# Performance work log

Measured on AMD Instinct MI355X. Metric: run time of the kernel, lower is better.

Reference implementation:

```python
import jax, jax.numpy as jnp
import numpy as np

B, C, H, W = 32, 128, 64, 64
D = 256          # attn_unit_dim
FF = 512         # ffn latent dim (2.0 * 256, rounded to /16*16)
NL = 2           # n_attn_blocks
PH = PW = 2      # patch size
EPS = 1e-5


def _cf_ln(x, g, b):
    # channel-first LayerNorm over dim 1 (unbiased=False variance)
    m = jnp.mean(x, axis=1, keepdims=True)
    v = jnp.mean((x - m) ** 2, axis=1, keepdims=True)
    return (x - m) * jax.lax.rsqrt(v + EPS) * g.reshape(1, -1, 1, 1) + b.reshape(1, -1, 1, 1)


def _conv1x1(x, w, b=None):
    y = jnp.einsum('bcpq,dc->bdpq', x, w)
    return y if b is None else y + b.reshape(1, -1, 1, 1)


def _bn(x, g, b, m, v):
    # eval-mode BatchNorm2d with running stats
    return (x - m.reshape(1, -1, 1, 1)) * jax.lax.rsqrt(v.reshape(1, -1, 1, 1) + EPS) \
        * g.reshape(1, -1, 1, 1) + b.reshape(1, -1, 1, 1)


def setup_inputs() -> dict:
    key = jax.random.key(0)
    ks = iter(jax.random.split(key, 64))
    rn = lambda shape, s=0.02: jax.random.normal(next(ks), shape, jnp.float32) * s
    pv = lambda shape: 1.0 + 0.1 * jax.random.uniform(next(ks), shape, jnp.float32)
    return {
        'x': jax.random.normal(next(ks), (B, C, H, W), jnp.float32),
        # local_rep: depthwise 3x3 + BN + leaky_relu, then 1x1 -> D
        'dw_w': rn((C, 1, 3, 3), 0.1),
        'bn1_g': pv((C,)), 'bn1_b': rn((C,), 0.1),
        'bn1_m': rn((C,), 0.1), 'bn1_v': pv((C,)),
        'c1_w': rn((D, C)), 'c1_b': rn((D,), 0.01),
        # per-layer transformer params (stacked over NL)
        'ln1_g': pv((NL, D)), 'ln1_b': rn((NL, D), 0.1),
        'qkv_w': rn((NL, 1 + 2 * D, D)), 'qkv_b': rn((NL, 1 + 2 * D), 0.01),
        'out_w': rn((NL, D, D)), 'out_b': rn((NL, D), 0.01),
        'ln2_g': pv((NL, D)), 'ln2_b': rn((NL, D), 0.1),
        'f1_w': rn((NL, FF, D)), 'f1_b': rn((NL, FF), 0.01),
        'f2_w': rn((NL, D, FF)), 'f2_b': rn((NL, D), 0.01),
        'lnf_g': pv((D,)), 'lnf_b': rn((D,), 0.1),
        # conv_proj: 1x1 (no bias) + BN
        'proj_w': rn((C, D)),
        'bn2_g': pv((C,)), 'bn2_b': rn((C,), 0.1),
        'bn2_m': rn((C,), 0.1), 'bn2_v': pv((C,)),
    }


def reference(x, dw_w, bn1_g, bn1_b, bn1_m, bn1_v, c1_w, c1_b,
              ln1_g, ln1_b, qkv_w, qkv_b, out_w, out_b,
              ln2_g, ln2_b, f1_w, f1_b, f2_w, f2_b,
              lnf_g, lnf_b, proj_w, bn2_g, bn2_b, bn2_m, bn2_v):
    # local representation: depthwise 3x3 conv + BN + leaky_relu(0.1) + 1x1 conv
    y = jax.lax.conv_general_dilated(
        x, dw_w, window_strides=(1, 1), padding=[(1, 1), (1, 1)],
        dimension_numbers=('NCHW', 'OIHW', 'NCHW'), feature_group_count=C)
    y = _bn(y, bn1_g, bn1_b, bn1_m, bn1_v)
    y = jax.nn.leaky_relu(y, 0.1)
    y = _conv1x1(y, c1_w, c1_b)                       # [B, D, H, W]

    # unfold -> [B, D, P, N], P = PH*PW pixels/patch, N = patches
    nh, nw = H // PH, W // PW
    p = y.reshape(B, D, nh, PH, nw, PW).transpose(0, 1, 3, 5, 2, 4).reshape(B, D, PH * PW, nh * nw)

    # global representation: NL pre-norm linear-attention transformer blocks
    for l in range(NL):
        z = _cf_ln(p, ln1_g[l], ln1_b[l])
        qkv = _conv1x1(z, qkv_w[l], qkv_b[l])          # [B, 1+2D, P, N]
        q, k, v = qkv[:, :1], qkv[:, 1:1 + D], qkv[:, 1 + D:]
        scores = jax.nn.softmax(q, axis=-1)            # softmax over patches N
        ctx = jnp.sum(k * scores, axis=-1, keepdims=True)  # [B, D, P, 1]
        attn = _conv1x1(jax.nn.relu(v) * ctx, out_w[l], out_b[l])
        p = p + attn
        z = _cf_ln(p, ln2_g[l], ln2_b[l])
        h = jax.nn.leaky_relu(_conv1x1(z, f1_w[l], f1_b[l]), 0.1)
        p = p + _conv1x1(h, f2_w[l], f2_b[l])
    p = _cf_ln(p, lnf_g, lnf_b)

    # fold back -> [B, D, H, W]
    fm = p.reshape(B, D, PH, PW, nh, nw).transpose(0, 1, 4, 2, 5, 3).reshape(B, D, H, W)

    # conv_proj: 1x1 (no bias) + BN -> [B, C, H, W]
    fm = _conv1x1(fm, proj_w)
    fm = _bn(fm, bn2_g, bn2_b, bn2_m, bn2_v)
    return fm
```

## Files before the change

kernel.cpp:

```cpp
#include <hip/hip_runtime.h>


typedef short  bh8 __attribute__((ext_vector_type(8)));
typedef float  f4  __attribute__((ext_vector_type(4)));
typedef unsigned short us2 __attribute__((ext_vector_type(2)));
typedef unsigned short us4 __attribute__((ext_vector_type(4)));

constexpr int Bc = 32, Cc = 128, Dc = 256, FFc = 512;
constexpr int NNc = 1024, Sc = 4096;
constexpr float EPSc = 1e-5f;

enum SrcMode { S_LNF32, S_BF16 };
enum OutMode { O_STOREF32, O_FOLDBN };

__device__ __forceinline__ unsigned short f2bf(float f) {
  union { float f; unsigned int u; } v; v.f = f;
  unsigned int u = v.u + 0x7FFFu + ((v.u >> 16) & 1u);
  return (unsigned short)(u >> 16);
}

__global__ __launch_bounds__(256) void k_wconv(
    const float* __restrict__ w, unsigned short* __restrict__ dst,
    int total, int klog2)
{
// ... 49 lines not shown
  *reinterpret_cast<us2*>(y1 + base + (ph * 2 + 0) * NNc) = (us2){r[0], r[2]};
  *reinterpret_cast<us2*>(y1 + base + (ph * 2 + 1) * NNc) = (us2){r[1], r[3]};
}

template<bool QD>
__global__ __launch_bounds__(256) void k_lnstats(
    const float* __restrict__ p, const float* __restrict__ wgq,
    float* __restrict__ mean_, float* __restrict__ rstd_, float* __restrict__ qdot)
{
  __shared__ float wg_s[256];
  int t = threadIdx.x;
  if (QD) { wg_s[t] = wgq[t]; __syncthreads(); }
  int pos = blockIdx.x * 256 + t;
  int b = pos >> 12, s = pos & 4095;
  const float* base = p + (size_t)b * Dc * Sc + s;
  float sum = 0.f, sq = 0.f, qa = 0.f;
  for (int d = 0; d < Dc; ++d) {
    float v = base[(size_t)d * Sc];
    sum += v; sq += v * v;
    if (QD) qa += v * wg_s[d];
  }
  float m   = sum * (1.f / Dc);
  float var = sq * (1.f / Dc) - m * m;
  mean_[pos] = m;
  rstd_[pos] = rsqrtf(fmaxf(var, 0.f) + EPSc);
  if (QD) qdot[pos] = qa;
}

__global__ void k_prep(const float* __restrict__ wq, const float* __restrict__ lng,
                       const float* __restrict__ lnb, const float* __restrict__ qb,
                       float* __restrict__ wgq, float* __restrict__ scal)
{
  int t = threadIdx.x, lane = t & 63, wv = t >> 6;
  float w = wq[t];
  float a = w * lng[t], c2 = w * lnb[t];
  wgq[t] = a;
  __shared__ float ra[4], rb[4];
  #pragma unroll
  for (int off = 32; off > 0; off >>= 1) { a += __shfl_xor(a, off); c2 += __shfl_xor(c2, off); }
  if (lane == 0) { ra[wv] = a; rb[wv] = c2; }
  __syncthreads();
  if (t == 0) {
    scal[0] = ra[0] + ra[1] + ra[2] + ra[3];
    scal[1] = rb[0] + rb[1] + rb[2] + rb[3] + qb[0];
  }
}

__global__ __launch_bounds__(256) void k_softmax2(
    const float* __restrict__ qdot, const float* __restrict__ mean_,
    const float* __restrict__ rstd_, const float* __restrict__ scal,
    float* __restrict__ ub, float* __restrict__ Ub)
{
  int bp = blockIdx.x, b = bp >> 2, pp = bp & 3;
  int t = threadIdx.x, lane = t & 63, wv = t >> 6;
  __shared__ float r3[4], r4[4];
  float s1 = scal[0], s2 = scal[1];
  int pos0 = b * Sc + pp * NNc;
  float q[4], m_r[4], rs_r[4];
  float mx = -3.4e38f;
  #pragma unroll
  for (int i = 0; i < 4; ++i) {
    int pos = pos0 + t + i * 256;
    m_r[i] = mean_[pos]; rs_r[i] = rstd_[pos];
    q[i] = rs_r[i] * qdot[pos] - m_r[i] * rs_r[i] * s1 + s2;
    mx = fmaxf(mx, q[i]);
  }
  #pragma unroll
  for (int off = 32; off > 0; off >>= 1) mx = fmaxf(mx, __shfl_xor(mx, off));
  if (lane == 0) r3[wv] = mx;
  __syncthreads();
  mx = fmaxf(fmaxf(r3[0], r3[1]), fmaxf(r3[2], r3[3]));
  float sum = 0.f;
  #pragma unroll
  for (int i = 0; i < 4; ++i) { q[i] = __expf(q[i] - mx); sum += q[i]; }
  #pragma unroll
  for (int off = 32; off > 0; off >>= 1) sum += __shfl_xor(sum, off);
  if (lane == 0) r4[wv] = sum;
  __syncthreads();
  float inv = 1.f / (r4[0] + r4[1] + r4[2] + r4[3]);
  float pU = 0.f;
  #pragma unroll
  for (int i = 0; i < 4; ++i) {
    float un = rs_r[i] * q[i] * inv;
    ub[(size_t)bp * NNc + t + i * 256] = un;
    pU += m_r[i] * un;
  }
  #pragma unroll
  for (int off = 32; off > 0; off >>= 1) pU += __shfl_xor(pU, off);
  if (lane == 0) r3[wv] = pU;
  __syncthreads();
  if (t == 0) Ub[bp] = r3[0] + r3[1] + r3[2] + r3[3];
}

__global__ __launch_bounds__(256) void k_tpass(
    const float* __restrict__ p, const float* __restrict__ ub,
    const float* __restrict__ Ub, const float* __restrict__ lng,
    const float* __restrict__ lnb, float* __restrict__ tb)
{
  int cs = blockIdx.x, pp = blockIdx.y, b = blockIdx.z;
  int bp = b * 4 + pp;
  int t = threadIdx.x, lane = t & 63, wv = t >> 6;
  __shared__ float u_s[1024];
  for (int i = t; i < 1024; i += 256) u_s[i] = ub[(size_t)bp * NNc + i];
  __syncthreads();
  float U = Ub[bp];
  const float* pb = p + (size_t)b * Dc * Sc + pp * NNc;
  for (int i = 0; i < 16; ++i) {
    int c = cs * 64 + wv * 16 + i;
    const float* row = pb + (size_t)c * Sc;
    float sm = 0.f;
    #pragma unroll
    for (int j = 0; j < 16; ++j) { int n = lane + 64 * j; sm += row[n] * u_s[n]; }
    #pragma unroll
    for (int off = 32; off > 0; off >>= 1) sm += __shfl_xor(sm, off);
    if (lane == 0) tb[(size_t)bp * Dc + c] = lng[c] * (sm - U) + lnb[c];
  }
}

__global__ __launch_bounds__(256) void k_ctx2(
    const float* __restrict__ tb, const float* __restrict__ wk,
    const float* __restrict__ bk, float* __restrict__ ctxb)
{
  int b = blockIdx.x, d = threadIdx.x;
  __shared__ float ts[4][256];
  for (int i = threadIdx.x; i < 1024; i += 256) ts[i >> 8][i & 255] = tb[(size_t)b * 1024 + i];
  __syncthreads();
  const float* wrow = wk + (size_t)d * 256;
  float bkd = bk[d];
  float accp[4] = {0.f, 0.f, 0.f, 0.f};
  for (int c = 0; c < 256; c += 4) {
    float4 wv = *reinterpret_cast<const float4*>(wrow + c);
    #pragma unroll
    for (int pp = 0; pp < 4; ++pp)
      accp[pp] += wv.x * ts[pp][c] + wv.y * ts[pp][c + 1]
                + wv.z * ts[pp][c + 2] + wv.w * ts[pp][c + 3];
  }
  #pragma unroll
  for (int pp = 0; pp < 4; ++pp)
    ctxb[((size_t)(b * 256 + d)) * 4 + pp] = accp[pp] + bkd;
}

__global__ void k_bn2pre(const float* __restrict__ g, const float* __restrict__ bb,
                         const float* __restrict__ mm, const float* __restrict__ vv,
                         float* __restrict__ sc, float* __restrict__ sh)
{
  int c = threadIdx.x;
  if (c < Cc) {
    float s = g[c] * rsqrtf(vv[c] + EPSc);
    sc[c] = s;
    sh[c] = bb[c] - mm[c] * s;
  }
}

template<int M1, bool ATTN, bool QDOT>
__global__ __launch_bounds__(256) void k_fused(
    const float* __restrict__ p,
    const float* __restrict__ mean_, const float* __restrict__ rstd_,
    const float* __restrict__ lng, const float* __restrict__ lnb,
    const unsigned short* __restrict__ wf1, const float* __restrict__ b1,
    const float* __restrict__ ctxp,
    const unsigned short* __restrict__ wf2, const float* __restrict__ b2,
    float* __restrict__ dst,
    const float* __restrict__ wgq2,
    float* __restrict__ mean_o, float* __restrict__ rstd_o,
    float* __restrict__ qdot_o)
{
  constexpr int NT = 32;
  constexpr int NF = NT / 16;
  constexpr int ACC1 = M1 / 64;
  int t = threadIdx.x;
  int wv = t >> 6, lane = t & 63;
  int q = lane >> 4, ln16 = lane & 15;
  int nt = blockIdx.x, pp = blockIdx.y, b = blockIdx.z;
  int n0 = nt * NT;

  __shared__ unsigned int Alds[2][NT * 20];
  __shared__ unsigned short Frag[M1 * NT];
  __shared__ float m_s[NT], rs_s[NT];
  __shared__ float ctx_s[ATTN ? 256 : 4];

  int kp_s = t >> 4;
  int n2_s = (t & 15) * 2;

  size_t pbase = (size_t)b * Dc * Sc + pp * NNc + n0;

  float2 c0 = *reinterpret_cast<const float2*>(p + pbase + (size_t)(kp_s * 2) * Sc + n2_s);
  float2 c1 = *reinterpret_cast<const float2*>(p + pbase + (size_t)(kp_s * 2 + 1) * Sc + n2_s);

  if (t < NT) {
    int pos = b * Sc + pp * NNc + n0 + t;
    m_s[t]  = mean_[pos];
    rs_s[t] = rstd_[pos];
  }
  if (ATTN) ctx_s[t] = ctxp[(size_t)(b * Dc + t) * 4 + pp];

  f4 acc[ACC1][NF];
  #pragma unroll
  for (int i = 0; i < ACC1; ++i)
    #pragma unroll
    for (int j = 0; j < NF; ++j) acc[i][j] = (f4){0.f, 0.f, 0.f, 0.f};

  __syncthreads();

  for (int kc = 0; kc < 256; kc += 32) {
    int k0 = kc + kp_s * 2;
    float g0 = lng[k0], g1 = lng[k0 + 1];
    float h0 = lnb[k0], h1 = lnb[k0 + 1];
    float ms0 = m_s[n2_s],     rs0 = rs_s[n2_s];
    float ms1 = m_s[n2_s + 1], rs1 = rs_s[n2_s + 1];
    float a00 = (c0.x - ms0) * rs0 * g0 + h0;
    float a01 = (c0.y - ms1) * rs1 * g0 + h0;
    float a10 = (c1.x - ms0) * rs0 * g1 + h1;
    float a11 = (c1.y - ms1) * rs1 * g1 + h1;
    unsigned int pk0 = (unsigned int)f2bf(a00) | ((unsigned int)f2bf(a10) << 16);
    unsigned int pk1 = (unsigned int)f2bf(a01) | ((unsigned int)f2bf(a11) << 16);

    if (kc < 224) {
      c0 = *reinterpret_cast<const float2*>(p + pbase + (size_t)(kc + 32 + kp_s * 2) * Sc + n2_s);
      c1 = *reinterpret_cast<const float2*>(p + pbase + (size_t)(kc + 32 + kp_s * 2 + 1) * Sc + n2_s);
    }

    unsigned int* alw = Alds[(kc >> 5) & 1];
    alw[n2_s * 20 + kp_s]       = pk0;
    alw[(n2_s + 1) * 20 + kp_s] = pk1;

    bh8 aw[ACC1];
    #pragma unroll
    for (int tm = 0; tm < ACC1; ++tm)
      aw[tm] = *(const bh8*)(wf1 + ((size_t)((kc >> 5) * (M1 >> 4) + wv * ACC1 + tm) * 64 + lane) * 8);

    __syncthreads();

    const unsigned short* al = (const unsigned short*)Alds[(kc >> 5) & 1];
    #pragma unroll
    for (int tn = 0; tn < NF; ++tn) {
      bh8 bwf = *(const bh8*)(al + (tn * 16 + ln16) * 40 + q * 8);
      #pragma unroll
      for (int tm = 0; tm < ACC1; ++tm)
        acc[tm][tn] = __builtin_amdgcn_mfma_f32_16x16x32_bf16(aw[tm], bwf, acc[tm][tn], 0, 0, 0);
    }
  }

  #pragma unroll
  for (int tm = 0; tm < ACC1; ++tm) {
    int row0 = wv * (M1 / 4) + tm * 16 + q * 4;
    float bia[4], cxv[4];
    #pragma unroll
    for (int r = 0; r < 4; ++r) {
      bia[r] = b1[row0 + r];
      if (ATTN) cxv[r] = ctx_s[row0 + r];
    }
    int kt  = row0 >> 5;
    int sub = (row0 >> 3) & 3;
    int jo  = row0 & 7;
    #pragma unroll
    for (int tn = 0; tn < NF; ++tn) {
      int cl = tn * 16 + ln16;
      us4 pk;
      #pragma unroll
      for (int r = 0; r < 4; ++r) {
        float v = acc[tm][tn][r] + bia[r];
        if (ATTN) v = fmaxf(v, 0.f) * cxv[r];
        else      v = v > 0.f ? v : 0.1f * v;
        pk[r] = f2bf(v);
      }
      *reinterpret_cast<us4*>(Frag + (((kt * NF + (cl >> 4)) * 64 + (sub << 4 | (cl & 15))) * 8 + jo)) = pk;
    }
  }
  __syncthreads();

  f4 acc2[4][NF];
  #pragma unroll
  for (int i = 0; i < 4; ++i)
    #pragma unroll
    for (int j = 0; j < NF; ++j) acc2[i][j] = (f4){0.f, 0.f, 0.f, 0.f};

  for (int kc = 0; kc < M1; kc += 32) {
    bh8 aw2[4];
    #pragma unroll
    for (int tm = 0; tm < 4; ++tm)
      aw2[tm] = *(const bh8*)(wf2 + ((size_t)((kc >> 5) * 16 + wv * 4 + tm) * 64 + lane) * 8);
    #pragma unroll
    for (int tn = 0; tn < NF; ++tn) {
      bh8 bwf = *(const bh8*)(Frag + ((kc >> 5) * NF + tn) * 512 + lane * 8);
      #pragma unroll
      for (int tm = 0; tm < 4; ++tm)
        acc2[tm][tn] = __builtin_amdgcn_mfma_f32_16x16x32_bf16(aw2[tm], bwf, acc2[tm][tn], 0, 0, 0);
    }
  }

  float s1[NF], s2[NF], s3[NF];
  #pragma unroll
  for (int tn = 0; tn < NF; ++tn) { s1[tn] = 0.f; s2[tn] = 0.f; s3[tn] = 0.f; }
  #pragma unroll
  for (int tm = 0; tm < 4; ++tm) {
    #pragma unroll
    for (int r = 0; r < 4; ++r) {
      int row = wv * 64 + tm * 16 + q * 4 + r;
      float bv = b2[row];
      float wqr = QDOT ? wgq2[row] : 0.f;
      #pragma unroll
      for (int tn = 0; tn < NF; ++tn) {
        int col = n0 + tn * 16 + ln16;
        size_t da = (size_t)(b * Dc + row) * Sc + pp * NNc + col;
        float v = dst[da] + acc2[tm][tn][r] + bv;
        dst[da] = v;
        s1[tn] += v; s2[tn] += v * v;
        if (QDOT) s3[tn] += v * wqr;
      }
    }
  }
  #pragma unroll
  for (int tn = 0; tn < NF; ++tn) {
    s1[tn] += __shfl_xor(s1[tn], 16); s1[tn] += __shfl_xor(s1[tn], 32);
    s2[tn] += __shfl_xor(s2[tn], 16); s2[tn] += __shfl_xor(s2[tn], 32);
    if (QDOT) { s3[tn] += __shfl_xor(s3[tn], 16); s3[tn] += __shfl_xor(s3[tn], 32); }
  }
  __syncthreads();
  float* fr = (float*)Frag;
  if (q == 0) {
    #pragma unroll
    for (int tn = 0; tn < NF; ++tn) {
      int col = tn * 16 + ln16;
      fr[(wv * 3 + 0) * NT + col] = s1[tn];
      fr[(wv * 3 + 1) * NT + col] = s2[tn];
      fr[(wv * 3 + 2) * NT + col] = s3[tn];
    }
  }
  __syncthreads();
  if (t < NT) {
    float a1 = 0.f, a2 = 0.f, a3 = 0.f;
    #pragma unroll
    for (int w2 = 0; w2 < 4; ++w2) {
      a1 += fr[(w2 * 3 + 0) * NT + t];
      a2 += fr[(w2 * 3 + 1) * NT + t];
      a3 += fr[(w2 * 3 + 2) * NT + t];
    }
    int pos = b * Sc + pp * NNc + n0 + t;
    float mn  = a1 * (1.f / 256.f);
    float var = a2 * (1.f / 256.f) - mn * mn;
    mean_o[pos] = mn;
    rstd_o[pos] = rsqrtf(fmaxf(var, 0.f) + EPSc);
    if (QDOT) qdot_o[pos] = a3;
  }
}

template<int KTOT, int MTOT, int SRCCH, int SSTR, bool SPP,
         SrcMode SM, OutMode OM>
__global__ __launch_bounds__(256) void k_mm(
    const void* __restrict__ src,
    const float* __restrict__ mean_, const float* __restrict__ rstd_,
    const float* __restrict__ lng, const float* __restrict__ lnb,
    const unsigned short* __restrict__ wf, const float* __restrict__ bias,
    const float* __restrict__ bnsc, const float* __restrict__ bnsh,
    void* __restrict__ dst)
{
  int t = threadIdx.x;
  int wv = t >> 6, lane = t & 63;
  int wm = wv & 1, wn = wv >> 1;
  int q = lane >> 4, ln16 = lane & 15;
  int nb = blockIdx.x, b = blockIdx.z;
  int pp = blockIdx.y & 3, mb = blockIdx.y >> 2;
  int n0  = nb * 128;
  int MB0 = mb * 128;

  __shared__ unsigned int Alds[128 * 20];
  __shared__ float m_s[128], rs_s[128];

  if (SM == S_LNF32 && t < 128) {
    int pos = b * Sc + pp * NNc + n0 + t;
    m_s[t]  = mean_[pos];
    rs_s[t] = rstd_[pos];
  }

  f4 acc[4][4];
  #pragma unroll
  for (int i = 0; i < 4; ++i)
    #pragma unroll
    for (int j = 0; j < 4; ++j) acc[i][j] = (f4){0.f, 0.f, 0.f, 0.f};

  size_t sbase = (size_t)b * SRCCH * SSTR + pp * NNc + n0;
  int mtb = (MB0 >> 4) + wm * 4;

  for (int kc = 0; kc < KTOT; kc += 32) {
    bh8 aw[4];
    #pragma unroll
    for (int tm = 0; tm < 4; ++tm)
      aw[tm] = *(const bh8*)(wf + ((size_t)((kc >> 5) * (MTOT >> 4) + mtb + tm) * 64 + lane) * 8);
    __syncthreads();
    #pragma unroll
    for (int it = 0; it < 8; ++it) {
      int n_l = (t & 63) + (it & 1) * 64;
      int kp  = (t >> 6) + (it >> 1) * 4;
      int k0  = kc + kp * 2;
      unsigned int pk;
      if (SM == S_LNF32) {
        const float* sp = (const float*)src;
        float a0 = sp[sbase + (size_t)k0 * SSTR + n_l];
        float a1 = sp[sbase + (size_t)(k0 + 1) * SSTR + n_l];
        float ms = m_s[n_l], rs = rs_s[n_l];
        a0 = (a0 - ms) * rs * lng[k0] + lnb[k0];
        a1 = (a1 - ms) * rs * lng[k0 + 1] + lnb[k0 + 1];
        pk = (unsigned int)f2bf(a0) | ((unsigned int)f2bf(a1) << 16);
      } else {
        const unsigned short* sp = (const unsigned short*)src;
        unsigned int u0 = sp[sbase + (size_t)k0 * SSTR + n_l];
        unsigned int u1 = sp[sbase + (size_t)(k0 + 1) * SSTR + n_l];
        pk = u0 | (u1 << 16);
      }
      Alds[n_l * 20 + kp] = pk;
    }
    __syncthreads();
    const unsigned short* al = (const unsigned short*)Alds;
    #pragma unroll
    for (int tn = 0; tn < 4; ++tn) {
      int nrow = wn * 64 + tn * 16 + ln16;
      bh8 bwf = *(const bh8*)(al + nrow * 40 + q * 8);
      #pragma unroll
      for (int tm = 0; tm < 4; ++tm)
        acc[tm][tn] = __builtin_amdgcn_mfma_f32_16x16x32_bf16(aw[tm], bwf, acc[tm][tn], 0, 0, 0);
    }
  }

  #pragma unroll
  for (int tm = 0; tm < 4; ++tm) {
    #pragma unroll
    for (int r = 0; r < 4; ++r) {
      int row = MB0 + wm * 64 + tm * 16 + q * 4 + r;
      float scv = 0.f, shv = 0.f, bv = 0.f;
      if (OM == O_FOLDBN) { scv = bnsc[row]; shv = bnsh[row]; }
      else                { bv = bias[row]; }
      #pragma unroll
      for (int tn = 0; tn < 4; ++tn) {
        int col = n0 + wn * 64 + tn * 16 + ln16;
        float v = acc[tm][tn][r];
        if (OM == O_FOLDBN) {
          int hh = 2 * (col >> 5) + (pp >> 1), ww = 2 * (col & 31) + (pp & 1);
          ((float*)dst)[((size_t)(b * Cc + row)) * Sc + hh * 64 + ww] = v * scv + shv;
        } else {
          ((float*)dst)[(size_t)(b * MTOT + row) * Sc + pp * NNc + col] = v + bv;
        }
      }
    }
  }
}

extern "C" void kernel_launch(void* const* d_in, const int* in_sizes, int n_in,
                              void* d_out, int out_size, void* d_ws, size_t ws_size,
                              hipStream_t stream)
{
  const float* x     = (const float*)d_in[0];
  const float* dw_w  = (const float*)d_in[1];
  const float* bn1_g = (const float*)d_in[2];
  const float* bn1_b = (const float*)d_in[3];
  const float* bn1_m = (const float*)d_in[4];
  const float* bn1_v = (const float*)d_in[5];
  const float* c1_w  = (const float*)d_in[6];
  const float* c1_b  = (const float*)d_in[7];
  const float* ln1_g = (const float*)d_in[8];
  const float* ln1_b = (const float*)d_in[9];
  const float* qkv_w = (const float*)d_in[10];
  const float* qkv_b = (const float*)d_in[11];
  const float* out_w = (const float*)d_in[12];
  const float* out_b = (const float*)d_in[13];
  const float* ln2_g = (const float*)d_in[14];
  const float* ln2_b = (const float*)d_in[15];
  const float* f1_w  = (const float*)d_in[16];
  const float* f1_b  = (const float*)d_in[17];
  const float* f2_w  = (const float*)d_in[18];
  const float* f2_b  = (const float*)d_in[19];
  const float* lnf_g = (const float*)d_in[20];
  const float* lnf_b = (const float*)d_in[21];
  const float* projw = (const float*)d_in[22];
  const float* bn2_g = (const float*)d_in[23];
  const float* bn2_b = (const float*)d_in[24];
  const float* bn2_m = (const float*)d_in[25];
  const float* bn2_v = (const float*)d_in[26];
  float* out = (float*)d_out;

  float* ws    = (float*)d_ws;
  float* p     = ws;
  float* reg   = p + (size_t)33554432;
  unsigned short* y1u = (unsigned short*)reg;
  float* mean2 = reg;
  float* rstd2 = reg + 131072;
  float* meanb = reg   + (size_t)8388608;
  float* rstdb = meanb + 131072;
  float* qdotb = rstdb + 131072;
  float* ub    = qdotb + 131072;
  float* Ub    = ub    + 131072;
  float* tb    = Ub    + 128;
  float* ctxb  = tb    + 32768;
  float* wgq   = ctxb  + 32768;
  float* scal  = wgq   + 512;
  float* bnscb = scal  + 16;
  float* bnshb = bnscb + 128;
  unsigned short* wfb = (unsigned short*)(bnshb + 128);
  unsigned short* wf_c1   = wfb;
  unsigned short* wf_v0   = wfb + 32768;
  unsigned short* wf_proj = wfb + 32768 + 2 * 393216;

  k_wconv<<<128, 256, 0, stream>>>(c1_w, wf_c1, 256 * 128, 7);
  for (int l = 0; l < 2; ++l) {
    const float* wvp = qkv_w + ((size_t)l * 513 + 257) * Dc;
    unsigned short* base = wf_v0 + (size_t)l * 393216;
    k_wconv<<<256, 256, 0, stream>>>(wvp, base, 256 * 256, 8);
    k_wconv<<<256, 256, 0, stream>>>(out_w + (size_t)l * Dc * Dc, base + 65536, 256 * 256, 8);
    k_wconv<<<512, 256, 0, stream>>>(f1_w + (size_t)l * FFc * Dc, base + 131072, 512 * 256, 8);
    k_wconv<<<512, 256, 0, stream>>>(f2_w + (size_t)l * Dc * FFc, base + 262144, 256 * 512, 9);
  }
  k_wconv<<<128, 256, 0, stream>>>(projw, wf_proj, 128 * 256, 8);

  for (int l = 0; l < 2; ++l)
    k_prep<<<1, 256, 0, stream>>>(qkv_w + (size_t)l * 513 * Dc,
                                  ln1_g + l * Dc, ln1_b + l * Dc,
                                  qkv_b + l * 513, wgq + l * 256, scal + l * 2);

  k_dwconv<<<16384, 256, 0, stream>>>(x, dw_w, bn1_g, bn1_b, bn1_m, bn1_v, y1u);

  k_mm<128, 256, 128, 4096, true, S_BF16, O_STOREF32>
      <<<dim3(8, 8, 32), 256, 0, stream>>>(
      y1u, nullptr, nullptr, nullptr, nullptr, wf_c1, c1_b, nullptr, nullptr, p);

  k_lnstats<true><<<512, 256, 0, stream>>>(p, wgq, meanb, rstdb, qdotb);

  for (int l = 0; l < 2; ++l) {
    const float* g1 = ln1_g + l * Dc; const float* b1 = ln1_b + l * Dc;
    const float* g2 = ln2_g + l * Dc; const float* b2 = ln2_b + l * Dc;
    const float* wk = qkv_w + ((size_t)l * 513 + 1) * Dc;
    const float* bk = qkv_b + l * 513 + 1;
    const float* bvv = qkv_b + l * 513 + 257;
    unsigned short* wbase = wf_v0 + (size_t)l * 393216;

    k_softmax2<<<128, 256, 0, stream>>>(qdotb, meanb, rstdb, scal + l * 2, ub, Ub);
    k_tpass<<<dim3(4, 4, 32), 256, 0, stream>>>(p, ub, Ub, g1, b1, tb);
    k_ctx2<<<32, 256, 0, stream>>>(tb, wk, bk, ctxb);

    k_fused<256, true, false><<<dim3(32, 4, 32), 256, 0, stream>>>(
        p, meanb, rstdb, g1, b1, wbase, bvv, ctxb,
        wbase + 65536, out_b + l * Dc, p,
        nullptr, mean2, rstd2, nullptr);

    if (l == 0) {
      k_fused<512, false, true><<<dim3(32, 4, 32), 256, 0, stream>>>(
          p, mean2, rstd2, g2, b2, wbase + 131072, f1_b + l * FFc, nullptr,
          wbase + 262144, f2_b + l * Dc, p,
          wgq + 256, meanb, rstdb, qdotb);
    } else {
      k_fused<512, false, false><<<dim3(32, 4, 32), 256, 0, stream>>>(
          p, mean2, rstd2, g2, b2, wbase + 131072, f1_b + l * FFc, nullptr,
          wbase + 262144, f2_b + l * Dc, p,
          nullptr, meanb, rstdb, nullptr);
    }
  }

  k_bn2pre<<<1, 128, 0, stream>>>(bn2_g, bn2_b, bn2_m, bn2_v, bnscb, bnshb);
  k_mm<256, 128, 256, 4096, true, S_LNF32, O_FOLDBN>
      <<<dim3(8, 4, 32), 256, 0, stream>>>(
      p, meanb, rstdb, lnf_g, lnf_b, wf_proj, nullptr, bnscb, bnshb, out);
}
```

Measured before the change: 780.0 us.

## Widen fused MLP tile to 64 columns and stream hidden dim in slabs

```diff
diff --git a/kernel.cpp b/kernel.cpp
--- a/kernel.cpp
+++ b/kernel.cpp
@@ -226,7 +226,7 @@
 }
 
 template<int M1, bool ATTN, bool QDOT>
-__global__ __launch_bounds__(256) void k_fused(
+__global__ __launch_bounds__(256, 3) void k_fused(
     const float* __restrict__ p,
     const float* __restrict__ mean_, const float* __restrict__ rstd_,
     const float* __restrict__ lng, const float* __restrict__ lnb,
@@ -238,27 +238,32 @@
     float* __restrict__ mean_o, float* __restrict__ rstd_o,
     float* __restrict__ qdot_o)
 {
-  constexpr int NT = 32;
+  constexpr int NT = 64;
   constexpr int NF = NT / 16;
-  constexpr int ACC1 = M1 / 64;
+  constexpr int SLABS = M1 / 128;
   int t = threadIdx.x;
   int wv = t >> 6, lane = t & 63;
   int q = lane >> 4, ln16 = lane & 15;
   int nt = blockIdx.x, pp = blockIdx.y, b = blockIdx.z;
   int n0 = nt * NT;
 
-  __shared__ unsigned int Alds[2][NT * 20];
-  __shared__ unsigned short Frag[M1 * NT];
+  __shared__ unsigned int At[256 * NT / 2];
+  __shared__ unsigned short Frag[128 * NT];
   __shared__ float m_s[NT], rs_s[NT];
   __shared__ float ctx_s[ATTN ? 256 : 4];
 
-  int kp_s = t >> 4;
-  int n2_s = (t & 15) * 2;
-
   size_t pbase = (size_t)b * Dc * Sc + pp * NNc + n0;
 
-  float2 c0 = *reinterpret_cast<const float2*>(p + pbase + (size_t)(kp_s * 2) * Sc + n2_s);
-  float2 c1 = *reinterpret_cast<const float2*>(p + pbase + (size_t)(kp_s * 2 + 1) * Sc + n2_s);
+  int kp_s = (t >> 5) & 7;
+  int col  = (t & 31) * 2;
+
+  auto kof = [&](int it) { return ((it >> 1) << 5) + ((it & 1) << 4) + kp_s * 2; };
+
+  int ka = kof(0), kb = kof(1);
+  float2 a0 = *reinterpret_cast<const float2*>(p + pbase + (size_t)ka * Sc + col);
+  float2 a1 = *reinterpret_cast<const float2*>(p + pbase + (size_t)(ka + 1) * Sc + col);
+  float2 b0 = *reinterpret_cast<const float2*>(p + pbase + (size_t)kb * Sc + col);
+  float2 b1v = *reinterpret_cast<const float2*>(p + pbase + (size_t)(kb + 1) * Sc + col);
 
   if (t < NT) {
     int pos = b * Sc + pp * NNc + n0 + t;
@@ -266,99 +271,125 @@
     rs_s[t] = rstd_[pos];
   }
   if (ATTN) ctx_s[t] = ctxp[(size_t)(b * Dc + t) * 4 + pp];
-
-  f4 acc[ACC1][NF];
-  #pragma unroll
-  for (int i = 0; i < ACC1; ++i)
-    #pragma unroll
-    for (int j = 0; j < NF; ++j) acc[i][j] = (f4){0.f, 0.f, 0.f, 0.f};
-
-  __syncthreads();
-
-  for (int kc = 0; kc < 256; kc += 32) {
-    int k0 = kc + kp_s * 2;
-    float g0 = lng[k0], g1 = lng[k0 + 1];
-    float h0 = lnb[k0], h1 = lnb[k0 + 1];
-    float ms0 = m_s[n2_s],     rs0 = rs_s[n2_s];
-    float ms1 = m_s[n2_s + 1], rs1 = rs_s[n2_s + 1];
-    float a00 = (c0.x - ms0) * rs0 * g0 + h0;
-    float a01 = (c0.y - ms1) * rs1 * g0 + h0;
-    float a10 = (c1.x - ms0) * rs0 * g1 + h1;
-    float a11 = (c1.y - ms1) * rs1 * g1 + h1;
-    unsigned int pk0 = (unsigned int)f2bf(a00) | ((unsigned int)f2bf(a10) << 16);
-    unsigned int pk1 = (unsigned int)f2bf(a01) | ((unsigned int)f2bf(a11) << 16);
-
-    if (kc < 224) {
-      c0 = *reinterpret_cast<const float2*>(p + pbase + (size_t)(kc + 32 + kp_s * 2) * Sc + n2_s);
-      c1 = *reinterpret_cast<const float2*>(p + pbase + (size_t)(kc + 32 + kp_s * 2 + 1) * Sc + n2_s);
-    }
-
-    unsigned int* alw = Alds[(kc >> 5) & 1];
-    alw[n2_s * 20 + kp_s]       = pk0;
-    alw[(n2_s + 1) * 20 + kp_s] = pk1;
-
-    bh8 aw[ACC1];
-    #pragma unroll
-    for (int tm = 0; tm < ACC1; ++tm)
-      aw[tm] = *(const bh8*)(wf1 + ((size_t)((kc >> 5) * (M1 >> 4) + wv * ACC1 + tm) * 64 + lane) * 8);
+  __syncthreads();
+
+  float ms0 = m_s[col], rs0 = rs_s[col];
+  float ms1 = m_s[col + 1], rs1 = rs_s[col + 1];
+
+  auto wrA = [&](int k0, int cx, unsigned int pk) {
+    At[(((k0 >> 5) * 4 + (cx >> 4)) << 8) + ((((k0 >> 3) & 3) * 16 + (cx & 15)) << 2)
+       + ((k0 & 7) >> 1)] = pk;
+  };
+
+  #pragma unroll 2
+  for (int it = 0; it < 16; it += 2) {
+    {
+      int k0 = kof(it);
+      float g0 = lng[k0], g1 = lng[k0 + 1];
+      float h0 = lnb[k0], h1 = lnb[k0 + 1];
+      float v00 = (a0.x - ms0) * rs0 * g0 + h0;
+      float v01 = (a0.y - ms1) * rs1 * g0 + h0;
+      float v10 = (a1.x - ms0) * rs0 * g1 + h1;
+      float v11 = (a1.y - ms1) * rs1 * g1 + h1;
+      if (it + 2 < 16) {
+        int kn = kof(it + 2);
+        a0 = *reinterpret_cast<const float2*>(p + pbase + (size_t)kn * Sc + col);
+        a1 = *reinterpret_cast<const float2*>(p + pbase + (size_t)(kn + 1) * Sc + col);
+      }
+      wrA(k0, col,     (unsigned int)f2bf(v00) | ((unsigned int)f2bf(v10) << 16));
+      wrA(k0, col + 1, (unsigned int)f2bf(v01) | ((unsigned int)f2bf(v11) << 16));
+    }
+    {
+      int k0 = kof(it + 1);
+      float g0 = lng[k0], g1 = lng[k0 + 1];
+      float h0 = lnb[k0], h1 = lnb[k0 + 1];
+      float v00 = (b0.x - ms0) * rs0 * g0 + h0;
+      float v01 = (b0.y - ms1) * rs1 * g0 + h0;
+      float v10 = (b1v.x - ms0) * rs0 * g1 + h1;
+      float v11 = (b1v.y - ms1) * rs1 * g1 + h1;
+      if (it + 3 < 16) {
+        int kn = kof(it + 3);
+        b0  = *reinterpret_cast<const float2*>(p + pbase + (size_t)kn * Sc + col);
+        b1v = *reinterpret_cast<const float2*>(p + pbase + (size_t)(kn + 1) * Sc + col);
+      }
+      wrA(k0, col,     (unsigned int)f2bf(v00) | ((unsigned int)f2bf(v10) << 16));
+      wrA(k0, col + 1, (unsigned int)f2bf(v01) | ((unsigned int)f2bf(v11) << 16));
+    }
+  }
+  __syncthreads();
+
+  const unsigned short* Ats = (const unsigned short*)At;
+
+  f4 acc2[4][NF];
+  #pragma unroll
+  for (int i = 0; i < 4; ++i)
+    #pragma unroll
+    for (int j = 0; j < NF; ++j) acc2[i][j] = (f4){0.f, 0.f, 0.f, 0.f};
+
+  for (int s = 0; s < SLABS; ++s) {
+    f4 acc1[2][NF];
+    #pragma unroll
+    for (int i = 0; i < 2; ++i)
+      #pragma unroll
+      for (int j = 0; j < NF; ++j) acc1[i][j] = (f4){0.f, 0.f, 0.f, 0.f};
+
+    for (int kc = 0; kc < 256; kc += 32) {
+      bh8 aw[2];
+      #pragma unroll
+      for (int tm = 0; tm < 2; ++tm)
+        aw[tm] = *(const bh8*)(wf1 + ((size_t)((kc >> 5) * (M1 >> 4) + s * 8 + wv * 2 + tm) * 64 + lane) * 8);
+      #pragma unroll
+      for (int tn = 0; tn < NF; ++tn) {
+        bh8 bwf = *(const bh8*)(Ats + ((kc >> 5) * 4 + tn) * 512 + lane * 8);
+        #pragma unroll
+        for (int tm = 0; tm < 2; ++tm)
+          acc1[tm][tn] = __builtin_amdgcn_mfma_f32_16x16x32_bf16(aw[tm], bwf, acc1[tm][tn], 0, 0, 0);
+      }
+    }
 
     __syncthreads();
 
-    const unsigned short* al = (const unsigned short*)Alds[(kc >> 5) & 1];
-    #pragma unroll
-    for (int tn = 0; tn < NF; ++tn) {
-      bh8 bwf = *(const bh8*)(al + (tn * 16 + ln16) * 40 + q * 8);
-      #pragma unroll
-      for (int tm = 0; tm < ACC1; ++tm)
-        acc[tm][tn] = __builtin_amdgcn_mfma_f32_16x16x32_bf16(aw[tm], bwf, acc[tm][tn], 0, 0, 0);
-    }
-  }
-
-  #pragma unroll
-  for (int tm = 0; tm < ACC1; ++tm) {
-    int row0 = wv * (M1 / 4) + tm * 16 + q * 4;
-    float bia[4], cxv[4];
-    #pragma unroll
-    for (int r = 0; r < 4; ++r) {
-      bia[r] = b1[row0 + r];
-      if (ATTN) cxv[r] = ctx_s[row0 + r];
-    }
-    int kt  = row0 >> 5;
-    int sub = (row0 >> 3) & 3;
-    int jo  = row0 & 7;
-    #pragma unroll
-    for (int tn = 0; tn < NF; ++tn) {
-      int cl = tn * 16 + ln16;
-      us4 pk;
+    #pragma unroll
+    for (int tm = 0; tm < 2; ++tm) {
+      int row0l = wv * 32 + tm * 16 + q * 4;
+      int row0g = s * 128 + row0l;
+      float bia[4], cxv[4];
       #pragma unroll
       for (int r = 0; r < 4; ++r) {
-        float v = acc[tm][tn][r] + bia[r];
-        if (ATTN) v = fmaxf(v, 0.f) * cxv[r];
-        else      v = v > 0.f ? v : 0.1f * v;
-        pk[r] = f2bf(v);
-      }
-      *reinterpret_cast<us4*>(Frag + (((kt * NF + (cl >> 4)) * 64 + (sub << 4 | (cl & 15))) * 8 + jo)) = pk;
-    }
-  }
-  __syncthreads();
-
-  f4 acc2[4][NF];
-  #pragma unroll
-  for (int i = 0; i < 4; ++i)
-    #pragma unroll
-    for (int j = 0; j < NF; ++j) acc2[i][j] = (f4){0.f, 0.f, 0.f, 0.f};
-
-  for (int kc = 0; kc < M1; kc += 32) {
-    bh8 aw2[4];
-    #pragma unroll
-    for (int tm = 0; tm < 4; ++tm)
-      aw2[tm] = *(const bh8*)(wf2 + ((size_t)((kc >> 5) * 16 + wv * 4 + tm) * 64 + lane) * 8);
-    #pragma unroll
-    for (int tn = 0; tn < NF; ++tn) {
-      bh8 bwf = *(const bh8*)(Frag + ((kc >> 5) * NF + tn) * 512 + lane * 8);
+        bia[r] = b1[row0g + r];
+        if (ATTN) cxv[r] = ctx_s[row0g + r];
+      }
+      int kt2 = row0l >> 5;
+      int sub = (row0l >> 3) & 3;
+      int jo  = row0l & 7;
+      #pragma unroll
+      for (int tn = 0; tn < NF; ++tn) {
+        int cl = tn * 16 + ln16;
+        us4 pk;
+        #pragma unroll
+        for (int r = 0; r < 4; ++r) {
+          float v = acc1[tm][tn][r] + bia[r];
+          if (ATTN) v = fmaxf(v, 0.f) * cxv[r];
+          else      v = v > 0.f ? v : 0.1f * v;
+          pk[r] = f2bf(v);
+        }
+        *reinterpret_cast<us4*>(Frag + (((kt2 * 4 + (cl >> 4)) * 64 + ((sub << 4) | (cl & 15))) * 8 + jo)) = pk;
+      }
+    }
+    __syncthreads();
+
+    for (int kc2 = 0; kc2 < 4; ++kc2) {
+      bh8 aw2[4];
       #pragma unroll
       for (int tm = 0; tm < 4; ++tm)
-        acc2[tm][tn] = __builtin_amdgcn_mfma_f32_16x16x32_bf16(aw2[tm], bwf, acc2[tm][tn], 0, 0, 0);
+        aw2[tm] = *(const bh8*)(wf2 + ((size_t)((s * 4 + kc2) * 16 + wv * 4 + tm) * 64 + lane) * 8);
+      #pragma unroll
+      for (int tn = 0; tn < NF; ++tn) {
+        bh8 bwf = *(const bh8*)(Frag + ((kc2 * 4 + tn) * 512) + lane * 8);
+        #pragma unroll
+        for (int tm = 0; tm < 4; ++tm)
+          acc2[tm][tn] = __builtin_amdgcn_mfma_f32_16x16x32_bf16(aw2[tm], bwf, acc2[tm][tn], 0, 0, 0);
+      }
     }
   }
 
@@ -374,8 +405,8 @@
       float wqr = QDOT ? wgq2[row] : 0.f;
       #pragma unroll
       for (int tn = 0; tn < NF; ++tn) {
-        int col = n0 + tn * 16 + ln16;
-        size_t da = (size_t)(b * Dc + row) * Sc + pp * NNc + col;
+        int cx = n0 + tn * 16 + ln16;
+        size_t da = (size_t)(b * Dc + row) * Sc + pp * NNc + cx;
         float v = dst[da] + acc2[tm][tn][r] + bv;
         dst[da] = v;
         s1[tn] += v; s2[tn] += v * v;
@@ -394,27 +425,27 @@
   if (q == 0) {
     #pragma unroll
     for (int tn = 0; tn < NF; ++tn) {
-      int col = tn * 16 + ln16;
-      fr[(wv * 3 + 0) * NT + col] = s1[tn];
-      fr[(wv * 3 + 1) * NT + col] = s2[tn];
-      fr[(wv * 3 + 2) * NT + col] = s3[tn];
+      int cx = tn * 16 + ln16;
+      fr[(wv * 3 + 0) * NT + cx] = s1[tn];
+      fr[(wv * 3 + 1) * NT + cx] = s2[tn];
+      fr[(wv * 3 + 2) * NT + cx] = s3[tn];
     }
   }
   __syncthreads();
   if (t < NT) {
-    float a1 = 0.f, a2 = 0.f, a3 = 0.f;
+    float a1s = 0.f, a2s = 0.f, a3s = 0.f;
     #pragma unroll
     for (int w2 = 0; w2 < 4; ++w2) {
-      a1 += fr[(w2 * 3 + 0) * NT + t];
-      a2 += fr[(w2 * 3 + 1) * NT + t];
-      a3 += fr[(w2 * 3 + 2) * NT + t];
+      a1s += fr[(w2 * 3 + 0) * NT + t];
+      a2s += fr[(w2 * 3 + 1) * NT + t];
+      a3s += fr[(w2 * 3 + 2) * NT + t];
     }
     int pos = b * Sc + pp * NNc + n0 + t;
-    float mn  = a1 * (1.f / 256.f);
-    float var = a2 * (1.f / 256.f) - mn * mn;
+    float mn  = a1s * (1.f / 256.f);
+    float var = a2s * (1.f / 256.f) - mn * mn;
     mean_o[pos] = mn;
     rstd_o[pos] = rsqrtf(fmaxf(var, 0.f) + EPSc);
-    if (QDOT) qdot_o[pos] = a3;
+    if (QDOT) qdot_o[pos] = a3s;
   }
 }
 
@@ -609,18 +640,18 @@
     k_tpass<<<dim3(4, 4, 32), 256, 0, stream>>>(p, ub, Ub, g1, b1, tb);
     k_ctx2<<<32, 256, 0, stream>>>(tb, wk, bk, ctxb);
 
-    k_fused<256, true, false><<<dim3(32, 4, 32), 256, 0, stream>>>(
+    k_fused<256, true, false><<<dim3(16, 4, 32), 256, 0, stream>>>(
         p, meanb, rstdb, g1, b1, wbase, bvv, ctxb,
         wbase + 65536, out_b + l * Dc, p,
         nullptr, mean2, rstd2, nullptr);
 
     if (l == 0) {
-      k_fused<512, false, true><<<dim3(32, 4, 32), 256, 0, stream>>>(
+      k_fused<512, false, true><<<dim3(16, 4, 32), 256, 0, stream>>>(
           p, mean2, rstd2, g2, b2, wbase + 131072, f1_b + l * FFc, nullptr,
           wbase + 262144, f2_b + l * Dc, p,
           wgq + 256, meanb, rstdb, qdotb);
     } else {
-      k_fused<512, false, false><<<dim3(32, 4, 32), 256, 0, stream>>>(
+      k_fused<512, false, false><<<dim3(16, 4, 32), 256, 0, stream>>>(
           p, mean2, rstd2, g2, b2, wbase + 131072, f1_b + l * FFc, nullptr,
           wbase + 262144, f2_b + l * Dc, p,
           nullptr, meanb, rstdb, nullptr);
```

Result: slower. 878.3 us (+12.6%).

## Fuse attention output projection and FFN into one kernel per layer

Applied to the files above, without the earlier changes.

```diff
diff --git a/kernel.cpp b/kernel.cpp
--- a/kernel.cpp
+++ b/kernel.cpp
@@ -225,22 +225,23 @@
   }
 }
 
-template<int M1, bool ATTN, bool QDOT>
-__global__ __launch_bounds__(256) void k_fused(
+template<bool QDOT>
+__global__ __launch_bounds__(256) void k_mega(
     const float* __restrict__ p,
     const float* __restrict__ mean_, const float* __restrict__ rstd_,
-    const float* __restrict__ lng, const float* __restrict__ lnb,
-    const unsigned short* __restrict__ wf1, const float* __restrict__ b1,
+    const float* __restrict__ g1, const float* __restrict__ b1,
+    const unsigned short* __restrict__ wfv, const float* __restrict__ bv,
     const float* __restrict__ ctxp,
-    const unsigned short* __restrict__ wf2, const float* __restrict__ b2,
+    const unsigned short* __restrict__ wfo, const float* __restrict__ bo,
+    const float* __restrict__ g2, const float* __restrict__ b2,
+    const unsigned short* __restrict__ wf1, const float* __restrict__ b1f,
+    const unsigned short* __restrict__ wf2, const float* __restrict__ b2f,
     float* __restrict__ dst,
     const float* __restrict__ wgq2,
     float* __restrict__ mean_o, float* __restrict__ rstd_o,
     float* __restrict__ qdot_o)
 {
-  constexpr int NT = 32;
-  constexpr int NF = NT / 16;
-  constexpr int ACC1 = M1 / 64;
+  constexpr int NT = 32, NF = 2;
   int t = threadIdx.x;
   int wv = t >> 6, lane = t & 63;
   int q = lane >> 4, ln16 = lane & 15;
@@ -248,14 +249,16 @@
   int n0 = nt * NT;
 
   __shared__ unsigned int Alds[2][NT * 20];
-  __shared__ unsigned short Frag[M1 * NT];
-  __shared__ float m_s[NT], rs_s[NT];
-  __shared__ float ctx_s[ATTN ? 256 : 4];
+  __shared__ unsigned short FragA[256 * NT];
+  __shared__ unsigned short FragF[128 * NT];
+  __shared__ float m_s[NT], rs_s[NT], m2_s[NT], rs2_s[NT];
+  __shared__ float ctx_s[256];
+  __shared__ float fr[12 * NT];
+
+  size_t pbase = (size_t)b * Dc * Sc + pp * NNc + n0;
 
   int kp_s = t >> 4;
   int n2_s = (t & 15) * 2;
-
-  size_t pbase = (size_t)b * Dc * Sc + pp * NNc + n0;
 
   float2 c0 = *reinterpret_cast<const float2*>(p + pbase + (size_t)(kp_s * 2) * Sc + n2_s);
   float2 c1 = *reinterpret_cast<const float2*>(p + pbase + (size_t)(kp_s * 2 + 1) * Sc + n2_s);
@@ -265,26 +268,26 @@
     m_s[t]  = mean_[pos];
     rs_s[t] = rstd_[pos];
   }
-  if (ATTN) ctx_s[t] = ctxp[(size_t)(b * Dc + t) * 4 + pp];
-
-  f4 acc[ACC1][NF];
-  #pragma unroll
-  for (int i = 0; i < ACC1; ++i)
-    #pragma unroll
-    for (int j = 0; j < NF; ++j) acc[i][j] = (f4){0.f, 0.f, 0.f, 0.f};
+  ctx_s[t] = ctxp[(size_t)(b * Dc + t) * 4 + pp];
+
+  f4 acc1a[4][NF];
+  #pragma unroll
+  for (int i = 0; i < 4; ++i)
+    #pragma unroll
+    for (int j = 0; j < NF; ++j) acc1a[i][j] = (f4){0.f, 0.f, 0.f, 0.f};
 
   __syncthreads();
 
   for (int kc = 0; kc < 256; kc += 32) {
     int k0 = kc + kp_s * 2;
-    float g0 = lng[k0], g1 = lng[k0 + 1];
-    float h0 = lnb[k0], h1 = lnb[k0 + 1];
+    float ga = g1[k0], gb = g1[k0 + 1];
+    float ha = b1[k0], hb = b1[k0 + 1];
     float ms0 = m_s[n2_s],     rs0 = rs_s[n2_s];
     float ms1 = m_s[n2_s + 1], rs1 = rs_s[n2_s + 1];
-    float a00 = (c0.x - ms0) * rs0 * g0 + h0;
-    float a01 = (c0.y - ms1) * rs1 * g0 + h0;
-    float a10 = (c1.x - ms0) * rs0 * g1 + h1;
-    float a11 = (c1.y - ms1) * rs1 * g1 + h1;
+    float a00 = (c0.x - ms0) * rs0 * ga + ha;
+    float a01 = (c0.y - ms1) * rs1 * ga + ha;
+    float a10 = (c1.x - ms0) * rs0 * gb + hb;
+    float a11 = (c1.y - ms1) * rs1 * gb + hb;
     unsigned int pk0 = (unsigned int)f2bf(a00) | ((unsigned int)f2bf(a10) << 16);
     unsigned int pk1 = (unsigned int)f2bf(a01) | ((unsigned int)f2bf(a11) << 16);
 
@@ -297,10 +300,10 @@
     alw[n2_s * 20 + kp_s]       = pk0;
     alw[(n2_s + 1) * 20 + kp_s] = pk1;
 
-    bh8 aw[ACC1];
-    #pragma unroll
-    for (int tm = 0; tm < ACC1; ++tm)
-      aw[tm] = *(const bh8*)(wf1 + ((size_t)((kc >> 5) * (M1 >> 4) + wv * ACC1 + tm) * 64 + lane) * 8);
+    bh8 aw[4];
+    #pragma unroll
+    for (int tm = 0; tm < 4; ++tm)
+      aw[tm] = *(const bh8*)(wfv + ((size_t)((kc >> 5) * 16 + wv * 4 + tm) * 64 + lane) * 8);
 
     __syncthreads();
 
@@ -309,19 +312,19 @@
     for (int tn = 0; tn < NF; ++tn) {
       bh8 bwf = *(const bh8*)(al + (tn * 16 + ln16) * 40 + q * 8);
       #pragma unroll
-      for (int tm = 0; tm < ACC1; ++tm)
-        acc[tm][tn] = __builtin_amdgcn_mfma_f32_16x16x32_bf16(aw[tm], bwf, acc[tm][tn], 0, 0, 0);
-    }
-  }
-
-  #pragma unroll
-  for (int tm = 0; tm < ACC1; ++tm) {
-    int row0 = wv * (M1 / 4) + tm * 16 + q * 4;
+      for (int tm = 0; tm < 4; ++tm)
+        acc1a[tm][tn] = __builtin_amdgcn_mfma_f32_16x16x32_bf16(aw[tm], bwf, acc1a[tm][tn], 0, 0, 0);
+    }
+  }
+
+  #pragma unroll
+  for (int tm = 0; tm < 4; ++tm) {
+    int row0 = wv * 64 + tm * 16 + q * 4;
     float bia[4], cxv[4];
     #pragma unroll
     for (int r = 0; r < 4; ++r) {
-      bia[r] = b1[row0 + r];
-      if (ATTN) cxv[r] = ctx_s[row0 + r];
+      bia[r] = bv[row0 + r];
+      cxv[r] = ctx_s[row0 + r];
     }
     int kt  = row0 >> 5;
     int sub = (row0 >> 3) & 3;
@@ -331,90 +334,231 @@
       int cl = tn * 16 + ln16;
       us4 pk;
       #pragma unroll
-      for (int r = 0; r < 4; ++r) {
-        float v = acc[tm][tn][r] + bia[r];
-        if (ATTN) v = fmaxf(v, 0.f) * cxv[r];
-        else      v = v > 0.f ? v : 0.1f * v;
-        pk[r] = f2bf(v);
-      }
-      *reinterpret_cast<us4*>(Frag + (((kt * NF + (cl >> 4)) * 64 + (sub << 4 | (cl & 15))) * 8 + jo)) = pk;
-    }
-  }
-  __syncthreads();
-
-  f4 acc2[4][NF];
+      for (int r = 0; r < 4; ++r)
+        pk[r] = f2bf(fmaxf(acc1a[tm][tn][r] + bia[r], 0.f) * cxv[r]);
+      *reinterpret_cast<us4*>(FragA + (((kt * NF + (cl >> 4)) * 64 + ((sub << 4) | (cl & 15))) * 8 + jo)) = pk;
+    }
+  }
+  __syncthreads();
+
+  f4 acc2a[4][NF];
   #pragma unroll
   for (int i = 0; i < 4; ++i)
     #pragma unroll
-    for (int j = 0; j < NF; ++j) acc2[i][j] = (f4){0.f, 0.f, 0.f, 0.f};
-
-  for (int kc = 0; kc < M1; kc += 32) {
+    for (int j = 0; j < NF; ++j) acc2a[i][j] = (f4){0.f, 0.f, 0.f, 0.f};
+
+  for (int kc = 0; kc < 256; kc += 32) {
     bh8 aw2[4];
     #pragma unroll
     for (int tm = 0; tm < 4; ++tm)
-      aw2[tm] = *(const bh8*)(wf2 + ((size_t)((kc >> 5) * 16 + wv * 4 + tm) * 64 + lane) * 8);
+      aw2[tm] = *(const bh8*)(wfo + ((size_t)((kc >> 5) * 16 + wv * 4 + tm) * 64 + lane) * 8);
     #pragma unroll
     for (int tn = 0; tn < NF; ++tn) {
-      bh8 bwf = *(const bh8*)(Frag + ((kc >> 5) * NF + tn) * 512 + lane * 8);
+      bh8 bwf = *(const bh8*)(FragA + ((kc >> 5) * NF + tn) * 512 + lane * 8);
       #pragma unroll
       for (int tm = 0; tm < 4; ++tm)
-        acc2[tm][tn] = __builtin_amdgcn_mfma_f32_16x16x32_bf16(aw2[tm], bwf, acc2[tm][tn], 0, 0, 0);
-    }
-  }
-
-  float s1[NF], s2[NF], s3[NF];
-  #pragma unroll
-  for (int tn = 0; tn < NF; ++tn) { s1[tn] = 0.f; s2[tn] = 0.f; s3[tn] = 0.f; }
+        acc2a[tm][tn] = __builtin_amdgcn_mfma_f32_16x16x32_bf16(aw2[tm], bwf, acc2a[tm][tn], 0, 0, 0);
+    }
+  }
+
   #pragma unroll
   for (int tm = 0; tm < 4; ++tm) {
     #pragma unroll
     for (int r = 0; r < 4; ++r) {
       int row = wv * 64 + tm * 16 + q * 4 + r;
-      float bv = b2[row];
+      float bvo = bo[row];
+      #pragma unroll
+      for (int tn = 0; tn < NF; ++tn) {
+        size_t da = pbase + (size_t)row * Sc + tn * 16 + ln16;
+        acc2a[tm][tn][r] = dst[da] + acc2a[tm][tn][r] + bvo;
+      }
+    }
+  }
+
+  {
+    float s1[NF] = {0.f, 0.f}, s2[NF] = {0.f, 0.f};
+    #pragma unroll
+    for (int tm = 0; tm < 4; ++tm)
+      #pragma unroll
+      for (int r = 0; r < 4; ++r)
+        #pragma unroll
+        for (int tn = 0; tn < NF; ++tn) {
+          float v = acc2a[tm][tn][r];
+          s1[tn] += v; s2[tn] += v * v;
+        }
+    #pragma unroll
+    for (int tn = 0; tn < NF; ++tn) {
+      s1[tn] += __shfl_xor(s1[tn], 16); s1[tn] += __shfl_xor(s1[tn], 32);
+      s2[tn] += __shfl_xor(s2[tn], 16); s2[tn] += __shfl_xor(s2[tn], 32);
+    }
+    __syncthreads();
+    if (q == 0) {
+      #pragma unroll
+      for (int tn = 0; tn < NF; ++tn) {
+        int cx = tn * 16 + ln16;
+        fr[(wv * 3 + 0) * NT + cx] = s1[tn];
+        fr[(wv * 3 + 1) * NT + cx] = s2[tn];
+      }
+    }
+    __syncthreads();
+    if (t < NT) {
+      float a1s = 0.f, a2s = 0.f;
+      #pragma unroll
+      for (int w2 = 0; w2 < 4; ++w2) {
+        a1s += fr[(w2 * 3 + 0) * NT + t];
+        a2s += fr[(w2 * 3 + 1) * NT + t];
+      }
+      float mn  = a1s * (1.f / 256.f);
+      float var = a2s * (1.f / 256.f) - mn * mn;
+      m2_s[t]  = mn;
+      rs2_s[t] = rsqrtf(fmaxf(var, 0.f) + EPSc);
+    }
+    __syncthreads();
+  }
+
+  {
+    unsigned int* At = (unsigned int*)FragA;
+    #pragma unroll
+    for (int tm = 0; tm < 4; ++tm) {
+      int k0 = wv * 64 + tm * 16 + q * 4;
+      float ga0 = g2[k0], ga1 = g2[k0 + 1], ga2 = g2[k0 + 2], ga3 = g2[k0 + 3];
+      float be0 = b2[k0], be1 = b2[k0 + 1], be2 = b2[k0 + 2], be3 = b2[k0 + 3];
+      int base0 = ((k0 >> 5) * 2) * 256 + (((k0 >> 3) & 3) * 16) * 4;
+      int w0i = (k0 & 7) >> 1;
+      #pragma unroll
+      for (int tn = 0; tn < NF; ++tn) {
+        int c = tn * 16 + ln16;
+        float mm = m2_s[c], rr = rs2_s[c];
+        float v0 = (acc2a[tm][tn][0] - mm) * rr * ga0 + be0;
+        float v1 = (acc2a[tm][tn][1] - mm) * rr * ga1 + be1;
+        float v2 = (acc2a[tm][tn][2] - mm) * rr * ga2 + be2;
+        float v3 = (acc2a[tm][tn][3] - mm) * rr * ga3 + be3;
+        int idx = base0 + (c >> 4) * 256 + (c & 15) * 4;
+        At[idx + w0i]     = (unsigned int)f2bf(v0) | ((unsigned int)f2bf(v1) << 16);
+        At[idx + w0i + 1] = (unsigned int)f2bf(v2) | ((unsigned int)f2bf(v3) << 16);
+      }
+    }
+  }
+  __syncthreads();
+
+  const unsigned short* Ats = FragA;
+  f4 acc2f[4][NF];
+  #pragma unroll
+  for (int i = 0; i < 4; ++i)
+    #pragma unroll
+    for (int j = 0; j < NF; ++j) acc2f[i][j] = (f4){0.f, 0.f, 0.f, 0.f};
+
+  for (int s = 0; s < 4; ++s) {
+    f4 acc1f[2][NF];
+    #pragma unroll
+    for (int i = 0; i < 2; ++i)
+      #pragma unroll
+      for (int j = 0; j < NF; ++j) acc1f[i][j] = (f4){0.f, 0.f, 0.f, 0.f};
+
+    for (int kc = 0; kc < 256; kc += 32) {
+      bh8 aw[2];
+      #pragma unroll
+      for (int tm = 0; tm < 2; ++tm)
+        aw[tm] = *(const bh8*)(wf1 + ((size_t)((kc >> 5) * 32 + s * 8 + wv * 2 + tm) * 64 + lane) * 8);
+      #pragma unroll
+      for (int tn = 0; tn < NF; ++tn) {
+        bh8 bwf = *(const bh8*)(Ats + ((kc >> 5) * 2 + tn) * 512 + lane * 8);
+        #pragma unroll
+        for (int tm = 0; tm < 2; ++tm)
+          acc1f[tm][tn] = __builtin_amdgcn_mfma_f32_16x16x32_bf16(aw[tm], bwf, acc1f[tm][tn], 0, 0, 0);
+      }
+    }
+
+    __syncthreads();
+
+    #pragma unroll
+    for (int tm = 0; tm < 2; ++tm) {
+      int row0l = wv * 32 + tm * 16 + q * 4;
+      int row0g = s * 128 + row0l;
+      float bia[4];
+      #pragma unroll
+      for (int r = 0; r < 4; ++r) bia[r] = b1f[row0g + r];
+      int kt2 = row0l >> 5;
+      int sub = (row0l >> 3) & 3;
+      int jo  = row0l & 7;
+      #pragma unroll
+      for (int tn = 0; tn < NF; ++tn) {
+        int cl = tn * 16 + ln16;
+        us4 pk;
+        #pragma unroll
+        for (int r = 0; r < 4; ++r) {
+          float v = acc1f[tm][tn][r] + bia[r];
+          pk[r] = f2bf(v > 0.f ? v : 0.1f * v);
+        }
+        *reinterpret_cast<us4*>(FragF + (((kt2 * 2 + (cl >> 4)) * 64 + ((sub << 4) | (cl & 15))) * 8 + jo)) = pk;
+      }
+    }
+    __syncthreads();
+
+    for (int kc2 = 0; kc2 < 4; ++kc2) {
+      bh8 aw2[4];
+      #pragma unroll
+      for (int tm = 0; tm < 4; ++tm)
+        aw2[tm] = *(const bh8*)(wf2 + ((size_t)((s * 4 + kc2) * 16 + wv * 4 + tm) * 64 + lane) * 8);
+      #pragma unroll
+      for (int tn = 0; tn < NF; ++tn) {
+        bh8 bwf = *(const bh8*)(FragF + (kc2 * 2 + tn) * 512 + lane * 8);
+        #pragma unroll
+        for (int tm = 0; tm < 4; ++tm)
+          acc2f[tm][tn] = __builtin_amdgcn_mfma_f32_16x16x32_bf16(aw2[tm], bwf, acc2f[tm][tn], 0, 0, 0);
+      }
+    }
+  }
+
+  float t1[NF] = {0.f, 0.f}, t2[NF] = {0.f, 0.f}, t3[NF] = {0.f, 0.f};
+  #pragma unroll
+  for (int tm = 0; tm < 4; ++tm) {
+    #pragma unroll
+    for (int r = 0; r < 4; ++r) {
+      int row = wv * 64 + tm * 16 + q * 4 + r;
+      float bvf = b2f[row];
       float wqr = QDOT ? wgq2[row] : 0.f;
       #pragma unroll
       for (int tn = 0; tn < NF; ++tn) {
-        int col = n0 + tn * 16 + ln16;
-        size_t da = (size_t)(b * Dc + row) * Sc + pp * NNc + col;
-        float v = dst[da] + acc2[tm][tn][r] + bv;
+        size_t da = pbase + (size_t)row * Sc + tn * 16 + ln16;
+        float v = acc2a[tm][tn][r] + acc2f[tm][tn][r] + bvf;
         dst[da] = v;
-        s1[tn] += v; s2[tn] += v * v;
-        if (QDOT) s3[tn] += v * wqr;
+        t1[tn] += v; t2[tn] += v * v;
+        if (QDOT) t3[tn] += v * wqr;
       }
     }
   }
   #pragma unroll
   for (int tn = 0; tn < NF; ++tn) {
-    s1[tn] += __shfl_xor(s1[tn], 16); s1[tn] += __shfl_xor(s1[tn], 32);
-    s2[tn] += __shfl_xor(s2[tn], 16); s2[tn] += __shfl_xor(s2[tn], 32);
-    if (QDOT) { s3[tn] += __shfl_xor(s3[tn], 16); s3[tn] += __shfl_xor(s3[tn], 32); }
-  }
-  __syncthreads();
-  float* fr = (float*)Frag;
+    t1[tn] += __shfl_xor(t1[tn], 16); t1[tn] += __shfl_xor(t1[tn], 32);
+    t2[tn] += __shfl_xor(t2[tn], 16); t2[tn] += __shfl_xor(t2[tn], 32);
+    if (QDOT) { t3[tn] += __shfl_xor(t3[tn], 16); t3[tn] += __shfl_xor(t3[tn], 32); }
+  }
+  __syncthreads();
   if (q == 0) {
     #pragma unroll
     for (int tn = 0; tn < NF; ++tn) {
-      int col = tn * 16 + ln16;
-      fr[(wv * 3 + 0) * NT + col] = s1[tn];
-      fr[(wv * 3 + 1) * NT + col] = s2[tn];
-      fr[(wv * 3 + 2) * NT + col] = s3[tn];
+      int cx = tn * 16 + ln16;
+      fr[(wv * 3 + 0) * NT + cx] = t1[tn];
+      fr[(wv * 3 + 1) * NT + cx] = t2[tn];
+      fr[(wv * 3 + 2) * NT + cx] = t3[tn];
     }
   }
   __syncthreads();
   if (t < NT) {
-    float a1 = 0.f, a2 = 0.f, a3 = 0.f;
+    float a1s = 0.f, a2s = 0.f, a3s = 0.f;
     #pragma unroll
     for (int w2 = 0; w2 < 4; ++w2) {
-      a1 += fr[(w2 * 3 + 0) * NT + t];
-      a2 += fr[(w2 * 3 + 1) * NT + t];
-      a3 += fr[(w2 * 3 + 2) * NT + t];
+      a1s += fr[(w2 * 3 + 0) * NT + t];
+      a2s += fr[(w2 * 3 + 1) * NT + t];
+      a3s += fr[(w2 * 3 + 2) * NT + t];
     }
     int pos = b * Sc + pp * NNc + n0 + t;
-    float mn  = a1 * (1.f / 256.f);
-    float var = a2 * (1.f / 256.f) - mn * mn;
+    float mn  = a1s * (1.f / 256.f);
+    float var = a2s * (1.f / 256.f) - mn * mn;
     mean_o[pos] = mn;
     rstd_o[pos] = rsqrtf(fmaxf(var, 0.f) + EPSc);
-    if (QDOT) qdot_o[pos] = a3;
+    if (QDOT) qdot_o[pos] = a3s;
   }
 }
 
@@ -555,8 +699,6 @@
   float* p     = ws;
   float* reg   = p + (size_t)33554432;
   unsigned short* y1u = (unsigned short*)reg;
-  float* mean2 = reg;
-  float* rstd2 = reg + 131072;
   float* meanb = reg   + (size_t)8388608;
   float* rstdb = meanb + 131072;
   float* qdotb = rstdb + 131072;
@@ -609,19 +751,18 @@
     k_tpass<<<dim3(4, 4, 32), 256, 0, stream>>>(p, ub, Ub, g1, b1, tb);
     k_ctx2<<<32, 256, 0, stream>>>(tb, wk, bk, ctxb);
 
-    k_fused<256, true, false><<<dim3(32, 4, 32), 256, 0, stream>>>(
-        p, meanb, rstdb, g1, b1, wbase, bvv, ctxb,
-        wbase + 65536, out_b + l * Dc, p,
-        nullptr, mean2, rstd2, nullptr);
-
     if (l == 0) {
-      k_fused<512, false, true><<<dim3(32, 4, 32), 256, 0, stream>>>(
-          p, mean2, rstd2, g2, b2, wbase + 131072, f1_b + l * FFc, nullptr,
+      k_mega<true><<<dim3(32, 4, 32), 256, 0, stream>>>(
+          p, meanb, rstdb, g1, b1,
+          wbase, bvv, ctxb, wbase + 65536, out_b + l * Dc,
+          g2, b2, wbase + 131072, f1_b + l * FFc,
           wbase + 262144, f2_b + l * Dc, p,
           wgq + 256, meanb, rstdb, qdotb);
     } else {
-      k_fused<512, false, false><<<dim3(32, 4, 32), 256, 0, stream>>>(
-          p, mean2, rstd2, g2, b2, wbase + 131072, f1_b + l * FFc, nullptr,
+      k_mega<false><<<dim3(32, 4, 32), 256, 0, stream>>>(
+          p, meanb, rstdb, g1, b1,
+          wbase, bvv, ctxb, wbase + 65536, out_b + l * Dc,
+          g2, b2, wbase + 131072, f1_b + l * FFc,
           wbase + 262144, f2_b + l * Dc, p,
           nullptr, meanb, rstdb, nullptr);
     }
```

After: 924.1 us. 1.18x slower.
